# Kernel tuning notes

Hardware: AMD Instinct MI355X
Metric: run time of the kernel (lower is better)

The kernel has to match this reference:

```python
import jax, jax.numpy as jnp
import numpy as np

N_NODES = 50000
N_EDGES = 800000
NFEAT, NHID, NCLASS = 256, 64, 2


def _deg_norm(idx, n_nodes, dtype):
    deg = jax.ops.segment_sum(jnp.ones(idx.shape[0], dtype=dtype), idx, num_segments=n_nodes)
    return jax.lax.rsqrt(jnp.maximum(deg, 1.0))


def gcn_layer(x, W, b, src, dst, n_nodes):
    # DGL GraphConv, norm='both': h = D_in^{-1/2} * Agg( D_out^{-1/2} * x ) W + b
    # weight applied before aggregation (in_feats >= out_feats path); math-equivalent.
    norm_src = _deg_norm(src, n_nodes, x.dtype)  # out-degree norm of source nodes
    norm_dst = _deg_norm(dst, n_nodes, x.dtype)  # in-degree norm of dest nodes
    h = (x * norm_src[:, None]) @ W              # [N, out]
    agg = jax.ops.segment_sum(h[src], dst, num_segments=n_nodes)  # gather + scatter-add
    return agg * norm_dst[:, None] + b


def setup_inputs() -> dict:
    key = jax.random.key(0)
    k1, k2, k3, k4, k5, k6, k7 = jax.random.split(key, 7)
    x = jax.random.normal(k1, (N_NODES, NFEAT), dtype=jnp.float32)
    src = jax.random.randint(k2, (N_EDGES,), 0, N_NODES, dtype=jnp.int64)
    dst = jax.random.randint(k3, (N_EDGES,), 0, N_NODES, dtype=jnp.int64)
    # Glorot-style init like DGL GraphConv
    W1 = jax.random.normal(k4, (NFEAT, NHID), dtype=jnp.float32) * (2.0 / (NFEAT + NHID)) ** 0.5
    b1 = jnp.zeros((NHID,), dtype=jnp.float32)
    W2 = jax.random.normal(k5, (NHID, NCLASS), dtype=jnp.float32) * (2.0 / (NHID + NCLASS)) ** 0.5
    b2 = jnp.zeros((NCLASS,), dtype=jnp.float32)
    return {"x": x, "src": src, "dst": dst, "W1": W1, "b1": b1, "W2": W2, "b2": b2}


def reference(x, src, dst, W1, b1, W2, b2):
    h = jax.nn.relu(gcn_layer(x, W1, b1, src, dst, N_NODES))
    # dropout=False -> p=0, no-op
    logits = gcn_layer(h, W2, b2, src, dst, N_NODES)
    return jax.nn.log_softmax(logits, axis=1)
```

## Files before the change

### kernel.cpp

```cpp
#include <hip/hip_runtime.h>
#include <math.h>

#define N_NODES 50000
#define N_EDGES 800000
#define NFEAT 256
#define NHID 64
#define NCLASS 2

#define DB 64
#define NDB 782
#define BCAP 1536
#define EPB 2048
#define NB_EDGE ((N_EDGES + EPB - 1) / EPB)

#define OFF_CURD 0
#define OFF_CURS 800
#define OFF_RBD  1600
#define OFF_NDST 101600
#define OFF_NSRC 151600
#define OFF_W1T  201600
#define OFF_DPK  209792
#define OFF_SV6  1410944
#define OFF_CSR  1711232
#define OFF_HB   2912384
#define OFF_H2   4512384

typedef __attribute__((ext_vector_type(8))) short bf16x8;
typedef __attribute__((ext_vector_type(8))) short short8;
typedef __attribute__((ext_vector_type(4))) float f32x4;

static __device__ __forceinline__ unsigned short f2bf(float f) {
    union { float f; unsigned int u; } v; v.f = f;
    return (unsigned short)((v.u + 0x8000u) >> 16);
}
static __device__ __forceinline__ unsigned int pk2bf(float f0, float f1) {
    union { float f; unsigned int u; } a, b; a.f = f0; b.f = f1;
    return __builtin_amdgcn_perm(b.u + 0x8000u, a.u + 0x8000u, 0x07060302u);
}
static __device__ __forceinline__ float bflo(unsigned int u) {
    union { unsigned int x; float f; } v; v.x = u << 16; return v.f;
}
static __device__ __forceinline__ float bfhi(unsigned int u) {
    union { unsigned int x; float f; } v; v.x = u & 0xffff0000u; return v.f;
}

#define INIT_N (1600 + NFEAT * NHID)
__global__ __launch_bounds__(256) void init_kernel(const float* __restrict__ W1,
                                                   int* __restrict__ cursors,
                                                   unsigned short* __restrict__ w1t) {
    int g = blockIdx.x * 256 + threadIdx.x;
    if (g < 1600) {
        cursors[g] = 0;
    } else if (g < INIT_N) {
        int idx = g - 1600;
        int k = idx >> 6, n = idx & 63;
        w1t[n * NFEAT + k] = f2bf(W1[idx]);
    }
}

__global__ __launch_bounds__(256) void bscatter_kernel(const int* __restrict__ src,
                                                       const int* __restrict__ dst,
                                                       int* __restrict__ cur_d,
                                                       int* __restrict__ cur_s,
                                                       int* __restrict__ dpk,
                                                       unsigned char* __restrict__ sv6) {
    __shared__ int hd[NDB], bd[NDB], cd[NDB], hs[NDB], bs[NDB], cs[NDB];
    int t = threadIdx.x;
    for (int i = t; i < NDB; i += 256) { hd[i] = 0; cd[i] = 0; hs[i] = 0; cs[i] = 0; }
    __syncthreads();
    int base = blockIdx.x * EPB;
    int ls[8], ld[8];
#pragma unroll
    for (int i = 0; i < 8; ++i) {
        int e = base + t + i * 256;
        ls[i] = (e < N_EDGES) ? src[e] : -1;
        ld[i] = (e < N_EDGES) ? dst[e] : -1;
        if (ld[i] >= 0) {
            atomicAdd(&hd[ld[i] >> 6], 1);
            atomicAdd(&hs[ls[i] >> 6], 1);
        }
    }
    __syncthreads();
    for (int i = t; i < NDB; i += 256) {
        if (hd[i]) bd[i] = atomicAdd(&cur_d[i], hd[i]);
        if (hs[i]) bs[i] = atomicAdd(&cur_s[i], hs[i]);
    }
    __syncthreads();
#pragma unroll
    for (int i = 0; i < 8; ++i) {
        if (ld[i] >= 0) {
            int bin = ld[i] >> 6;
            int pos = bd[bin] + atomicAdd(&cd[bin], 1);
            dpk[bin * BCAP + pos] = (ls[i] << 6) | (ld[i] & 63);
            int sbin = ls[i] >> 6;
            int spos = bs[sbin] + atomicAdd(&cs[sbin], 1);
            sv6[sbin * BCAP + spos] = (unsigned char)(ls[i] & 63);
        }
    }
}

union MidShared {
    struct { unsigned short As[64][136]; unsigned short Bs[64][136]; } g;
    struct { int ebuf[BCAP]; int hist4[256]; int hist[64]; int seg[64]; int cur[64]; } d;
    struct { int hist4[256]; } s;
};
__global__ __launch_bounds__(256) void mid_kernel(const int* __restrict__ cur_d,
                                                  const int* __restrict__ cur_s,
                                                  const int* __restrict__ dpk,
                                                  const unsigned char* __restrict__ sv6,
                                                  const float* __restrict__ x,
                                                  const unsigned short* __restrict__ w1t,
                                                  int2* __restrict__ rbdeg,
                                                  float* __restrict__ norm_dst,
                                                  float* __restrict__ norm_src,
                                                  int* __restrict__ csr,
                                                  unsigned short* __restrict__ hb) {
    __shared__ MidShared su;
    int t = threadIdx.x;
    int role = blockIdx.x % 3;
    int b = blockIdx.x / 3;

    if (role == 0) {
        su.s.hist4[t] = 0;
        __syncthreads();
        int cnt = cur_s[b];
        int base = b * BCAP;
        int sub = (t & 3) * 64;
        for (int j = t; j < cnt; j += 256) atomicAdd(&su.s.hist4[sub + sv6[base + j]], 1);
        __syncthreads();
        if (t < 64) {
            int gid = b * 64 + t;
            if (gid < N_NODES) {
                int v = su.s.hist4[t] + su.s.hist4[64 + t] + su.s.hist4[128 + t] + su.s.hist4[192 + t];
                norm_src[gid] = rsqrtf(fmaxf((float)v, 1.0f));
            }
        }
    } else if (role == 1) {
        int cnt = cur_d[b];
        int base = b * BCAP;
        if (t < 64) { su.d.hist[t] = 0; su.d.cur[t] = 0; }
        su.d.hist4[t] = 0;
        for (int j = t; j < cnt; j += 256) su.d.ebuf[j] = dpk[base + j];
        __syncthreads();
        int sub = (t & 3) * 64;
        for (int j = t; j < cnt; j += 256) atomicAdd(&su.d.hist4[sub + (su.d.ebuf[j] & 63)], 1);
        __syncthreads();
        if (t < 64) {
            int v = su.d.hist4[t] + su.d.hist4[64 + t] + su.d.hist4[128 + t] + su.d.hist4[192 + t];
            su.d.hist[t] = v;
            su.d.seg[t] = v;
        }
        __syncthreads();
#pragma unroll
        for (int off = 1; off < 64; off <<= 1) {
            int xv = 0;
            if (t < 64 && t >= off) xv = su.d.seg[t - off];
            __syncthreads();
            if (t < 64) su.d.seg[t] += xv;
            __syncthreads();
        }
        if (t < 64) {
            int v = su.d.hist[t];
            int excl = su.d.seg[t] - v;
            int gid = b * 64 + t;
            if (gid < N_NODES) {
                rbdeg[gid] = make_int2(base + excl, v);
                norm_dst[gid] = rsqrtf(fmaxf((float)v, 1.0f));
            }
            su.d.seg[t] = excl;
        }
        __syncthreads();
        for (int j = t; j < cnt; j += 256) {
            int p = su.d.ebuf[j];
            int dlow = p & 63;
            int pos = base + su.d.seg[dlow] + atomicAdd(&su.d.cur[dlow], 1);
            csr[pos] = ((unsigned)p) >> 6;
        }
    } else {
        const int row0 = b * 64;
        const int w = t >> 6;
        const int l = t & 63;
        const int m = l & 15;
        const int kq = (l >> 4) * 8;
        const int q = l >> 4;
        f32x4 acc[4] = {{0.f, 0.f, 0.f, 0.f}, {0.f, 0.f, 0.f, 0.f},
                        {0.f, 0.f, 0.f, 0.f}, {0.f, 0.f, 0.f, 0.f}};
#pragma unroll
        for (int half = 0; half < 2; ++half) {
            __syncthreads();
#pragma unroll
            for (int i = 0; i < 8; ++i) {
                int f = i * 256 + t;
                int r = f >> 5;
                int c4 = (f & 31) * 4;
                int grow = row0 + r;
                float4 av = make_float4(0.f, 0.f, 0.f, 0.f);
                if (grow < N_NODES)
                    av = *(const float4*)(&x[(size_t)grow * NFEAT + half * 128 + c4]);
                uint2 o;
                o.x = pk2bf(av.x, av.y);
                o.y = pk2bf(av.z, av.w);
                *(uint2*)(&su.g.As[r][c4]) = o;
            }
#pragma unroll
            for (int i = 0; i < 4; ++i) {
                int c = i * 256 + t;
                int n = c >> 4;
                int k8 = (c & 15) * 8;
                *(short8*)(&su.g.Bs[n][k8]) = *(const short8*)(&w1t[n * NFEAT + half * 128 + k8]);
            }
            __syncthreads();
#pragma unroll
            for (int c8 = 0; c8 < 4; ++c8) {
                int k0 = c8 * 32 + kq;
                bf16x8 a = *(const bf16x8*)(&su.g.As[w * 16 + m][k0]);
#pragma unroll
                for (int ct = 0; ct < 4; ++ct) {
                    bf16x8 bb = *(const bf16x8*)(&su.g.Bs[ct * 16 + m][k0]);
                    acc[ct] = __builtin_amdgcn_mfma_f32_16x16x32_bf16(a, bb, acc[ct], 0, 0, 0);
                }
            }
        }
#pragma unroll
        for (int reg = 0; reg < 4; ++reg) {
            int r = row0 + w * 16 + q * 4 + reg;
            if (r < N_NODES) {
#pragma unroll
                for (int ct = 0; ct < 4; ++ct)
                    hb[(size_t)r * NHID + ct * 16 + m] = f2bf(acc[ct][reg]);
            }
        }
    }
}

__global__ __launch_bounds__(256) void fused1_kernel(const int2* __restrict__ rbdeg,
                                                     const int* __restrict__ csr,
                                                     const unsigned short* __restrict__ hb,
                                                     const float* __restrict__ norm_dst,
                                                     const float* __restrict__ norm_src,
                                                     const float* __restrict__ b1,
                                                     const float* __restrict__ W2,
                                                     float* __restrict__ h2) {
    int gtid = blockIdx.x * blockDim.x + threadIdx.x;
    int node = gtid >> 6;
    int lane = gtid & 63;
    if (node >= N_NODES) return;
    int e8 = lane >> 3, fg = lane & 7;
    int2 rd = rbdeg[node];
    int beg = rd.x;
    int end = beg + rd.y;
    float a0 = 0.f, a1 = 0.f, a2 = 0.f, a3 = 0.f, a4 = 0.f, a5 = 0.f, a6 = 0.f, a7 = 0.f;
    for (int j = beg; j < end; j += 32) {
        int j0 = j + e8, j1 = j0 + 8, j2 = j0 + 16, j3 = j0 + 24;
        uint4 u0 = make_uint4(0u, 0u, 0u, 0u), u1 = make_uint4(0u, 0u, 0u, 0u);
        uint4 u2 = make_uint4(0u, 0u, 0u, 0u), u3 = make_uint4(0u, 0u, 0u, 0u);
        float ns0 = 0.f, ns1 = 0.f, ns2 = 0.f, ns3 = 0.f;
        if (j0 < end) {
            int s = csr[j0];
            ns0 = norm_src[s];
            u0 = *(const uint4*)(&hb[(size_t)s * NHID + fg * 8]);
        }
        if (j1 < end) {
            int s = csr[j1];
            ns1 = norm_src[s];
            u1 = *(const uint4*)(&hb[(size_t)s * NHID + fg * 8]);
        }
        if (j2 < end) {
            int s = csr[j2];
            ns2 = norm_src[s];
            u2 = *(const uint4*)(&hb[(size_t)s * NHID + fg * 8]);
        }
        if (j3 < end) {
            int s = csr[j3];
            ns3 = norm_src[s];
            u3 = *(const uint4*)(&hb[(size_t)s * NHID + fg * 8]);
        }
        a0 = fmaf(ns0, bflo(u0.x), fmaf(ns1, bflo(u1.x), fmaf(ns2, bflo(u2.x), fmaf(ns3, bflo(u3.x), a0))));
        a1 = fmaf(ns0, bfhi(u0.x), fmaf(ns1, bfhi(u1.x), fmaf(ns2, bfhi(u2.x), fmaf(ns3, bfhi(u3.x), a1))));
        a2 = fmaf(ns0, bflo(u0.y), fmaf(ns1, bflo(u1.y), fmaf(ns2, bflo(u2.y), fmaf(ns3, bflo(u3.y), a2))));
        a3 = fmaf(ns0, bfhi(u0.y), fmaf(ns1, bfhi(u1.y), fmaf(ns2, bfhi(u2.y), fmaf(ns3, bfhi(u3.y), a3))));
        a4 = fmaf(ns0, bflo(u0.z), fmaf(ns1, bflo(u1.z), fmaf(ns2, bflo(u2.z), fmaf(ns3, bflo(u3.z), a4))));
        a5 = fmaf(ns0, bfhi(u0.z), fmaf(ns1, bfhi(u1.z), fmaf(ns2, bfhi(u2.z), fmaf(ns3, bfhi(u3.z), a5))));
        a6 = fmaf(ns0, bflo(u0.w), fmaf(ns1, bflo(u1.w), fmaf(ns2, bflo(u2.w), fmaf(ns3, bflo(u3.w), a6))));
        a7 = fmaf(ns0, bfhi(u0.w), fmaf(ns1, bfhi(u1.w), fmaf(ns2, bfhi(u2.w), fmaf(ns3, bfhi(u3.w), a7))));
    }
#pragma unroll
    for (int off = 8; off <= 32; off <<= 1) {
        a0 += __shfl_xor(a0, off, 64);
        a1 += __shfl_xor(a1, off, 64);
        a2 += __shfl_xor(a2, off, 64);
        a3 += __shfl_xor(a3, off, 64);
        a4 += __shfl_xor(a4, off, 64);
        a5 += __shfl_xor(a5, off, 64);
        a6 += __shfl_xor(a6, off, 64);
        a7 += __shfl_xor(a7, off, 64);
    }
    float nd = norm_dst[node], ns = norm_src[node];
    float4 bv0 = *(const float4*)(&b1[fg * 8]);
    float4 bv1 = *(const float4*)(&b1[fg * 8 + 4]);
    float4 w0 = *(const float4*)(&W2[fg * 16 + 0]);
    float4 w1 = *(const float4*)(&W2[fg * 16 + 4]);
    float4 w2v = *(const float4*)(&W2[fg * 16 + 8]);
    float4 w3 = *(const float4*)(&W2[fg * 16 + 12]);
    float h0 = fmaxf(fmaf(a0, nd, bv0.x), 0.f) * ns;
    float h1 = fmaxf(fmaf(a1, nd, bv0.y), 0.f) * ns;
    float h2f = fmaxf(fmaf(a2, nd, bv0.z), 0.f) * ns;
    float h3 = fmaxf(fmaf(a3, nd, bv0.w), 0.f) * ns;
    float h4 = fmaxf(fmaf(a4, nd, bv1.x), 0.f) * ns;
    float h5 = fmaxf(fmaf(a5, nd, bv1.y), 0.f) * ns;
    float h6 = fmaxf(fmaf(a6, nd, bv1.z), 0.f) * ns;
    float h7 = fmaxf(fmaf(a7, nd, bv1.w), 0.f) * ns;
    float p0 = h0 * w0.x + h1 * w0.z + h2f * w1.x + h3 * w1.z +
               h4 * w2v.x + h5 * w2v.z + h6 * w3.x + h7 * w3.z;
    float p1 = h0 * w0.y + h1 * w0.w + h2f * w1.y + h3 * w1.w +
               h4 * w2v.y + h5 * w2v.w + h6 * w3.y + h7 * w3.w;
#pragma unroll
    for (int off = 1; off <= 4; off <<= 1) {
        p0 += __shfl_xor(p0, off, 64);
        p1 += __shfl_xor(p1, off, 64);
    }
    if (lane == 0) *(float2*)(&h2[node * 2]) = make_float2(p0, p1);
}

__global__ __launch_bounds__(256) void fused2_kernel(const int2* __restrict__ rbdeg,
                                                     const int* __restrict__ csr,
                                                     const float* __restrict__ h2,
                                                     const float* __restrict__ norm_dst,
                                                     const float* __restrict__ b2,
                                                     float* __restrict__ out) {
    int gtid = blockIdx.x * blockDim.x + threadIdx.x;
    int n = gtid >> 4;
    int l16 = gtid & 15;
    if (n >= N_NODES) return;
    int2 rd = rbdeg[n];
    int beg = rd.x, end = rd.x + rd.y;
    float s0 = 0.f, s1 = 0.f;
    for (int j = beg + l16; j < end; j += 16) {
        float2 v = *(const float2*)(&h2[csr[j] * 2]);
        s0 += v.x;
        s1 += v.y;
    }
#pragma unroll
    for (int off = 1; off <= 8; off <<= 1) {
        s0 += __shfl_xor(s0, off, 16);
        s1 += __shfl_xor(s1, off, 16);
    }
    if (l16 == 0) {
        float nd = norm_dst[n];
        float l0 = fmaf(s0, nd, b2[0]);
        float l1 = fmaf(s1, nd, b2[1]);
        float m = fmaxf(l0, l1);
        float lse = m + logf(expf(l0 - m) + expf(l1 - m));
        *(float2*)(&out[n * 2]) = make_float2(l0 - lse, l1 - lse);
    }
}

extern "C" void kernel_launch(void* const* d_in, const int* in_sizes, int n_in,
                              void* d_out, int out_size, void* d_ws, size_t ws_size,
                              hipStream_t stream) {
    const float* x  = (const float*)d_in[0];
    const int* src  = (const int*)d_in[1];
    const int* dst  = (const int*)d_in[2];
    const float* W1 = (const float*)d_in[3];
    const float* b1 = (const float*)d_in[4];
    const float* W2 = (const float*)d_in[5];
    const float* b2 = (const float*)d_in[6];
    float* out = (float*)d_out;
    float* ws  = (float*)d_ws;
    int*   wsi = (int*)d_ws;

    int*   cur_d    = wsi + OFF_CURD;
    int*   cur_s    = wsi + OFF_CURS;
    int2*  rbdeg    = (int2*)(wsi + OFF_RBD);
    float* norm_dst = ws + OFF_NDST;
    float* norm_src = ws + OFF_NSRC;
    unsigned short* w1t = (unsigned short*)(wsi + OFF_W1T);
    int*   dpk      = wsi + OFF_DPK;
    unsigned char* sv6 = (unsigned char*)(wsi + OFF_SV6);
    int*   csr      = wsi + OFF_CSR;
    unsigned short* hb = (unsigned short*)(wsi + OFF_HB);
    float* h2       = ws + OFF_H2;

    init_kernel<<<(INIT_N + 255) / 256, 256, 0, stream>>>(W1, cur_d, w1t);
    bscatter_kernel<<<NB_EDGE, 256, 0, stream>>>(src, dst, cur_d, cur_s, dpk, sv6);
    mid_kernel<<<NDB * 3, 256, 0, stream>>>(cur_d, cur_s, dpk, sv6, x, w1t,
                                            rbdeg, norm_dst, norm_src, csr, hb);
    {
        long long threads = (long long)N_NODES * 64;
        fused1_kernel<<<(int)((threads + 255) / 256), 256, 0, stream>>>(
            rbdeg, csr, hb, norm_dst, norm_src, b1, W2, h2);
    }
    {
        long long threads = (long long)N_NODES * 16;
        fused2_kernel<<<(int)((threads + 255) / 256), 256, 0, stream>>>(
            rbdeg, csr, h2, norm_dst, b2, out);
    }
}
```

Before: 177.9 us.

## Move GEMM into edge-scatter kernel and split CSR finalize into separate kernel

```diff
diff --git a/kernel.cpp b/kernel.cpp
--- a/kernel.cpp
+++ b/kernel.cpp
@@ -58,125 +58,55 @@
     }
 }
 
-__global__ __launch_bounds__(256) void bscatter_kernel(const int* __restrict__ src,
-                                                       const int* __restrict__ dst,
-                                                       int* __restrict__ cur_d,
-                                                       int* __restrict__ cur_s,
-                                                       int* __restrict__ dpk,
-                                                       unsigned char* __restrict__ sv6) {
-    __shared__ int hd[NDB], bd[NDB], cd[NDB], hs[NDB], bs[NDB], cs[NDB];
+union SgShared {
+    struct { int hd[NDB], bd[NDB], cd[NDB], hs[NDB], bs[NDB], cs[NDB]; } b;
+    struct { unsigned short As[64][136]; unsigned short Bs[64][136]; } g;
+};
+__global__ __launch_bounds__(256) void sg_kernel(const int* __restrict__ src,
+                                                 const int* __restrict__ dst,
+                                                 const float* __restrict__ x,
+                                                 const unsigned short* __restrict__ w1t,
+                                                 int* __restrict__ cur_d,
+                                                 int* __restrict__ cur_s,
+                                                 int* __restrict__ dpk,
+                                                 unsigned char* __restrict__ sv6,
+                                                 unsigned short* __restrict__ hb) {
+    __shared__ SgShared su;
     int t = threadIdx.x;
-    for (int i = t; i < NDB; i += 256) { hd[i] = 0; cd[i] = 0; hs[i] = 0; cs[i] = 0; }
-    __syncthreads();
-    int base = blockIdx.x * EPB;
-    int ls[8], ld[8];
-#pragma unroll
-    for (int i = 0; i < 8; ++i) {
-        int e = base + t + i * 256;
-        ls[i] = (e < N_EDGES) ? src[e] : -1;
-        ld[i] = (e < N_EDGES) ? dst[e] : -1;
-        if (ld[i] >= 0) {
-            atomicAdd(&hd[ld[i] >> 6], 1);
-            atomicAdd(&hs[ls[i] >> 6], 1);
-        }
-    }
-    __syncthreads();
-    for (int i = t; i < NDB; i += 256) {
-        if (hd[i]) bd[i] = atomicAdd(&cur_d[i], hd[i]);
-        if (hs[i]) bs[i] = atomicAdd(&cur_s[i], hs[i]);
-    }
-    __syncthreads();
-#pragma unroll
-    for (int i = 0; i < 8; ++i) {
-        if (ld[i] >= 0) {
-            int bin = ld[i] >> 6;
-            int pos = bd[bin] + atomicAdd(&cd[bin], 1);
-            dpk[bin * BCAP + pos] = (ls[i] << 6) | (ld[i] & 63);
-            int sbin = ls[i] >> 6;
-            int spos = bs[sbin] + atomicAdd(&cs[sbin], 1);
-            sv6[sbin * BCAP + spos] = (unsigned char)(ls[i] & 63);
-        }
-    }
-}
-
-union MidShared {
-    struct { unsigned short As[64][136]; unsigned short Bs[64][136]; } g;
-    struct { int ebuf[BCAP]; int hist4[256]; int hist[64]; int seg[64]; int cur[64]; } d;
-    struct { int hist4[256]; } s;
-};
-__global__ __launch_bounds__(256) void mid_kernel(const int* __restrict__ cur_d,
-                                                  const int* __restrict__ cur_s,
-                                                  const int* __restrict__ dpk,
-                                                  const unsigned char* __restrict__ sv6,
-                                                  const float* __restrict__ x,
-                                                  const unsigned short* __restrict__ w1t,
-                                                  int2* __restrict__ rbdeg,
-                                                  float* __restrict__ norm_dst,
-                                                  float* __restrict__ norm_src,
-                                                  int* __restrict__ csr,
-                                                  unsigned short* __restrict__ hb) {
-    __shared__ MidShared su;
-    int t = threadIdx.x;
-    int role = blockIdx.x % 3;
-    int b = blockIdx.x / 3;
-
-    if (role == 0) {
-        su.s.hist4[t] = 0;
-        __syncthreads();
-        int cnt = cur_s[b];
-        int base = b * BCAP;
-        int sub = (t & 3) * 64;
-        for (int j = t; j < cnt; j += 256) atomicAdd(&su.s.hist4[sub + sv6[base + j]], 1);
-        __syncthreads();
-        if (t < 64) {
-            int gid = b * 64 + t;
-            if (gid < N_NODES) {
-                int v = su.s.hist4[t] + su.s.hist4[64 + t] + su.s.hist4[128 + t] + su.s.hist4[192 + t];
-                norm_src[gid] = rsqrtf(fmaxf((float)v, 1.0f));
-            }
-        }
-    } else if (role == 1) {
-        int cnt = cur_d[b];
-        int base = b * BCAP;
-        if (t < 64) { su.d.hist[t] = 0; su.d.cur[t] = 0; }
-        su.d.hist4[t] = 0;
-        for (int j = t; j < cnt; j += 256) su.d.ebuf[j] = dpk[base + j];
-        __syncthreads();
-        int sub = (t & 3) * 64;
-        for (int j = t; j < cnt; j += 256) atomicAdd(&su.d.hist4[sub + (su.d.ebuf[j] & 63)], 1);
-        __syncthreads();
-        if (t < 64) {
-            int v = su.d.hist4[t] + su.d.hist4[64 + t] + su.d.hist4[128 + t] + su.d.hist4[192 + t];
-            su.d.hist[t] = v;
-            su.d.seg[t] = v;
-        }
-        __syncthreads();
-#pragma unroll
-        for (int off = 1; off < 64; off <<= 1) {
-            int xv = 0;
-            if (t < 64 && t >= off) xv = su.d.seg[t - off];
-            __syncthreads();
-            if (t < 64) su.d.seg[t] += xv;
-            __syncthreads();
-        }
-        if (t < 64) {
-            int v = su.d.hist[t];
-            int excl = su.d.seg[t] - v;
-            int gid = b * 64 + t;
-            if (gid < N_NODES) {
-                rbdeg[gid] = make_int2(base + excl, v);
-                norm_dst[gid] = rsqrtf(fmaxf((float)v, 1.0f));
-            }
-            su.d.seg[t] = excl;
-        }
-        __syncthreads();
-        for (int j = t; j < cnt; j += 256) {
-            int p = su.d.ebuf[j];
-            int dlow = p & 63;
-            int pos = base + su.d.seg[dlow] + atomicAdd(&su.d.cur[dlow], 1);
-            csr[pos] = ((unsigned)p) >> 6;
+    if (blockIdx.x < NB_EDGE) {
+        for (int i = t; i < NDB; i += 256) { su.b.hd[i] = 0; su.b.cd[i] = 0; su.b.hs[i] = 0; su.b.cs[i] = 0; }
+        __syncthreads();
+        int base = blockIdx.x * EPB;
+        int ls[8], ld[8];
+#pragma unroll
+        for (int i = 0; i < 8; ++i) {
+            int e = base + t + i * 256;
+            ls[i] = (e < N_EDGES) ? src[e] : -1;
+            ld[i] = (e < N_EDGES) ? dst[e] : -1;
+            if (ld[i] >= 0) {
+                atomicAdd(&su.b.hd[ld[i] >> 6], 1);
+                atomicAdd(&su.b.hs[ls[i] >> 6], 1);
+            }
+        }
+        __syncthreads();
+        for (int i = t; i < NDB; i += 256) {
+            if (su.b.hd[i]) su.b.bd[i] = atomicAdd(&cur_d[i], su.b.hd[i]);
+            if (su.b.hs[i]) su.b.bs[i] = atomicAdd(&cur_s[i], su.b.hs[i]);
+        }
+        __syncthreads();
+#pragma unroll
+        for (int i = 0; i < 8; ++i) {
+            if (ld[i] >= 0) {
+                int bin = ld[i] >> 6;
+                int pos = su.b.bd[bin] + atomicAdd(&su.b.cd[bin], 1);
+                dpk[bin * BCAP + pos] = (ls[i] << 6) | (ld[i] & 63);
+                int sbin = ls[i] >> 6;
+                int spos = su.b.bs[sbin] + atomicAdd(&su.b.cs[sbin], 1);
+                sv6[sbin * BCAP + spos] = (unsigned char)(ls[i] & 63);
+            }
         }
     } else {
+        const int b = blockIdx.x - NB_EDGE;
         const int row0 = b * 64;
         const int w = t >> 6;
         const int l = t & 63;
@@ -229,6 +159,82 @@
                 for (int ct = 0; ct < 4; ++ct)
                     hb[(size_t)r * NHID + ct * 16 + m] = f2bf(acc[ct][reg]);
             }
+        }
+    }
+}
+
+union FinShared {
+    struct { int ebuf[BCAP]; int hist4[256]; int hist[64]; int seg[64]; int cur[64]; } d;
+    struct { int hist4[256]; } s;
+};
+__global__ __launch_bounds__(256) void fin_kernel(const int* __restrict__ cur_d,
+                                                  const int* __restrict__ cur_s,
+                                                  const int* __restrict__ dpk,
+                                                  const unsigned char* __restrict__ sv6,
+                                                  int2* __restrict__ rbdeg,
+                                                  float* __restrict__ norm_dst,
+                                                  float* __restrict__ norm_src,
+                                                  int* __restrict__ csr) {
+    __shared__ FinShared su;
+    int t = threadIdx.x;
+    int role = blockIdx.x & 1;
+    int b = blockIdx.x >> 1;
+
+    if (role == 0) {
+        su.s.hist4[t] = 0;
+        __syncthreads();
+        int cnt = cur_s[b];
+        int base = b * BCAP;
+        int sub = (t & 3) * 64;
+        for (int j = t; j < cnt; j += 256) atomicAdd(&su.s.hist4[sub + sv6[base + j]], 1);
+        __syncthreads();
+        if (t < 64) {
+            int gid = b * 64 + t;
+            if (gid < N_NODES) {
+                int v = su.s.hist4[t] + su.s.hist4[64 + t] + su.s.hist4[128 + t] + su.s.hist4[192 + t];
+                norm_src[gid] = rsqrtf(fmaxf((float)v, 1.0f));
+            }
+        }
+    } else {
+        int cnt = cur_d[b];
+        int base = b * BCAP;
+        if (t < 64) { su.d.hist[t] = 0; su.d.cur[t] = 0; }
+        su.d.hist4[t] = 0;
+        for (int j = t; j < cnt; j += 256) su.d.ebuf[j] = dpk[base + j];
+        __syncthreads();
+        int sub = (t & 3) * 64;
+        for (int j = t; j < cnt; j += 256) atomicAdd(&su.d.hist4[sub + (su.d.ebuf[j] & 63)], 1);
+        __syncthreads();
+        if (t < 64) {
+            int v = su.d.hist4[t] + su.d.hist4[64 + t] + su.d.hist4[128 + t] + su.d.hist4[192 + t];
+            su.d.hist[t] = v;
+            su.d.seg[t] = v;
+        }
+        __syncthreads();
+#pragma unroll
+        for (int off = 1; off < 64; off <<= 1) {
+            int xv = 0;
+            if (t < 64 && t >= off) xv = su.d.seg[t - off];
+            __syncthreads();
+            if (t < 64) su.d.seg[t] += xv;
+            __syncthreads();
+        }
+        if (t < 64) {
+            int v = su.d.hist[t];
+            int excl = su.d.seg[t] - v;
+            int gid = b * 64 + t;
+            if (gid < N_NODES) {
+                rbdeg[gid] = make_int2(base + excl, v);
+                norm_dst[gid] = rsqrtf(fmaxf((float)v, 1.0f));
+            }
+            su.d.seg[t] = excl;
+        }
+        __syncthreads();
+        for (int j = t; j < cnt; j += 256) {
+            int p = su.d.ebuf[j];
+            int dlow = p & 63;
+            int pos = base + su.d.seg[dlow] + atomicAdd(&su.d.cur[dlow], 1);
+            csr[pos] = ((unsigned)p) >> 6;
         }
     }
 }
@@ -382,9 +388,8 @@
     float* h2       = ws + OFF_H2;
 
     init_kernel<<<(INIT_N + 255) / 256, 256, 0, stream>>>(W1, cur_d, w1t);
-    bscatter_kernel<<<NB_EDGE, 256, 0, stream>>>(src, dst, cur_d, cur_s, dpk, sv6);
-    mid_kernel<<<NDB * 3, 256, 0, stream>>>(cur_d, cur_s, dpk, sv6, x, w1t,
-                                            rbdeg, norm_dst, norm_src, csr, hb);
+    sg_kernel<<<NB_EDGE + NDB, 256, 0, stream>>>(src, dst, x, w1t, cur_d, cur_s, dpk, sv6, hb);
+    fin_kernel<<<NDB * 2, 256, 0, stream>>>(cur_d, cur_s, dpk, sv6, rbdeg, norm_dst, norm_src, csr);
     {
         long long threads = (long long)N_NODES * 64;
         fused1_kernel<<<(int)((threads + 255) / 256), 256, 0, stream>>>(
```

Measured after the change: 165.4 us. -7.0%, faster.
